# Performance work log

Hardware: AMD Instinct MI355X
Metric: run time of the kernel (lower is better)

## Reference

```python
import jax, jax.numpy as jnp
import numpy as np
from functools import partial

B, T, F = 4096, 256, 32
H1, H2, NT = 64, 32, 3


def _lstm_layer(x, W_ih, W_hh, b_ih, b_hh):
    """Torch-style LSTM (batch_first). x: [B,T,Fin], W_ih: [4H,Fin], W_hh: [4H,H].
    Gate order i, f, g, o. Returns all hidden states [B,T,H]."""
    Bsz = x.shape[0]
    H = W_hh.shape[1]
    # Precompute input contribution for all timesteps (one big GEMM)
    xg = jnp.einsum('btf,gf->btg', x, W_ih) + b_ih + b_hh  # [B,T,4H]

    def step(carry, xg_t):
        h, c = carry
        gates = xg_t + h @ W_hh.T  # [B,4H]
        i, f, g, o = jnp.split(gates, 4, axis=-1)
        i = jax.nn.sigmoid(i)
        f = jax.nn.sigmoid(f)
        g = jnp.tanh(g)
        o = jax.nn.sigmoid(o)
        c = f * c + i * g
        h = o * jnp.tanh(c)
        return (h, c), h

    init = (jnp.zeros((Bsz, H), x.dtype), jnp.zeros((Bsz, H), x.dtype))
    _, hs = jax.lax.scan(step, init, jnp.swapaxes(xg, 0, 1))  # hs: [T,B,H]
    return jnp.swapaxes(hs, 0, 1)


def setup_inputs() -> dict:
    key = jax.random.key(0)
    ks = jax.random.split(key, 12)
    s1 = 1.0 / np.sqrt(H1)
    s2 = 1.0 / np.sqrt(H2)
    u = lambda k, shape, s: jax.random.uniform(k, shape, jnp.float32, -s, s)
    return {
        'x': jax.random.normal(ks[0], (B, T, F), jnp.float32),
        'W_ih1': u(ks[1], (4 * H1, F), s1),
        'W_hh1': u(ks[2], (4 * H1, H1), s1),
        'b_ih1': u(ks[3], (4 * H1,), s1),
        'b_hh1': u(ks[4], (4 * H1,), s1),
        'W_ih2': u(ks[5], (4 * H2, H1), s2),
        'W_hh2': u(ks[6], (4 * H2, H2), s2),
        'b_ih2': u(ks[7], (4 * H2,), s2),
        'b_hh2': u(ks[8], (4 * H2,), s2),
        'W_head': u(ks[9], (NT, H2), s2),
        'b_head': u(ks[10], (NT,), s2),
    }


def reference(x, W_ih1, W_hh1, b_ih1, b_hh1, W_ih2, W_hh2, b_ih2, b_hh2, W_head, b_head):
    h1 = _lstm_layer(x, W_ih1, W_hh1, b_ih1, b_hh1)   # [B,T,64]; dropout is identity in eval
    h2 = _lstm_layer(h1, W_ih2, W_hh2, b_ih2, b_hh2)  # [B,T,32]
    last = h2[:, -1, :]                               # [B,32]
    return last @ W_head.T + b_head                   # [B,3]
```

## Files before the change

kernel.cpp:

```cpp
#include <hip/hip_runtime.h>

#define Bsz 4096
#define Tt  256
#define Ff  32
#define H1  64
#define H2  32
#define NTAPS 3
#define BT  8
#define NTHR 512
#define CH  16

typedef _Float16 half8  __attribute__((ext_vector_type(8)));
typedef __fp16   fp16x2 __attribute__((ext_vector_type(2)));
typedef float    f32x4  __attribute__((ext_vector_type(4)));

#define H1S 72
#define H2S 40
#define HDS 33

__device__ __forceinline__ float lstm_unit(float pi, float pf, float pg, float po,
                                           float& c) {
    const float K1 = 1.4426950408889634f;
    float ei = __builtin_amdgcn_exp2f(-K1 * pi);
    float ef = __builtin_amdgcn_exp2f(-K1 * pf);
    float eg = __builtin_amdgcn_exp2f(-2.0f * K1 * __builtin_fabsf(pg));
    float eo = __builtin_amdgcn_exp2f(-K1 * po);
    float p1 = (1.0f + ei) * (1.0f + eg);
    float pf1 = 1.0f + ef;
    float R  = __builtin_amdgcn_rcpf(p1 * pf1);
    float t1 = c * p1;
    float t2 = __builtin_copysignf(1.0f - eg, pg) * pf1;
    c = (t1 + t2) * R;
    float ec = __builtin_amdgcn_exp2f(-2.0f * K1 * __builtin_fabsf(c));
    float th = (1.0f - ec) * __builtin_amdgcn_rcpf((1.0f + eo) * (1.0f + ec));
    return __builtin_copysignf(th, c);
}

#define MFMA16(a, b, c) __builtin_amdgcn_mfma_f32_16x16x32_f16((a), (b), (c), 0, 0, 0)

__device__ __forceinline__ void dma16(const float* gp, const float* lp) {
    __builtin_amdgcn_global_load_lds(
        (const __attribute__((address_space(1))) void*)gp,
        (__attribute__((address_space(3))) void*)lp, 16, 0, 0);
}

__device__ __forceinline__ half8 cvt8(f32x4 lo, f32x4 hi) {
    union { half8 v; fp16x2 h[4]; } ax;
    ax.h[0] = __builtin_amdgcn_cvt_pkrtz(lo[0], lo[1]);
    ax.h[1] = __builtin_amdgcn_cvt_pkrtz(lo[2], lo[3]);
    ax.h[2] = __builtin_amdgcn_cvt_pkrtz(hi[0], hi[1]);
    ax.h[3] = __builtin_amdgcn_cvt_pkrtz(hi[2], hi[3]);
    return ax.v;
}

__global__ __launch_bounds__(NTHR, 2)
void lstm2_fused(const float* __restrict__ x,
                 const float* __restrict__ Wih1, const float* __restrict__ Whh1,
                 const float* __restrict__ bih1, const float* __restrict__ bhh1,
                 const float* __restrict__ Wih2, const float* __restrict__ Whh2,
                 const float* __restrict__ bih2, const float* __restrict__ bhh2,
                 const float* __restrict__ Whead, const float* __restrict__ bhead,
                 float* __restrict__ out)
{
    __shared__ __align__(16) _Float16 sH1[2][BT][H1S];
    __shared__ __align__(16) _Float16 sH2[2][BT][H2S];
    __shared__ __align__(16) float    sXC[2][CH][8][BT][4];
    __shared__ __align__(16) float    sHead[BT][HDS];

    const int tid  = threadIdx.x;
    const int wid  = tid >> 6;
    const int lane = tid & 63;
    const int l15  = lane & 15;
    const int q    = lane >> 4;
    const int row8 = l15 & 7;
    const int b0   = blockIdx.x * BT;
    const int u    = wid & 3;
    const bool isL1 = (wid < 4);

    const int colL1 = u * 16 + l15;
    const int r0  = (q >> 1) * 2, r1v = r0 + 1;
    const int bLo = (q & 1) * 4 + (q >> 1) * 2;
    const int hT = u & 1, rh = u >> 1;
    const int rL2 = (q >> 1) * 2 + rh;
    const int bL2 = (q & 1) * 4 + (q >> 1) * 2 + rh;

    const int bL  = lane & 7;
    const int f4L = lane >> 3;
    const float* gbase = x + (size_t)(b0 + bL) * Tt * Ff + f4L * 4;

    if (!isL1) {
        #pragma unroll
        for (int j = 0; j < 4; ++j) {
            int tl = u * 4 + j;
            dma16(gbase + (size_t)tl * Ff, &sXC[0][tl][0][0][0]);
        }
    }

    half8 wH[4][3];
    float bias[4];
    if (isL1) {
        #pragma unroll
        for (int G = 0; G < 4; ++G) {
            int gr = G * 64 + colL1;
            #pragma unroll
            for (int c = 0; c < 2; ++c) {
                half8 v;
                #pragma unroll
                for (int e = 0; e < 8; ++e)
                    v[e] = (_Float16)Whh1[gr * H1 + c * 32 + q * 8 + e];
                wH[G][c] = v;
            }
            half8 vx;
            #pragma unroll
            for (int e = 0; e < 8; ++e)
                vx[e] = (_Float16)Wih1[gr * Ff + q * 8 + e];
            wH[G][2] = vx;
            bias[G] = bih1[gr] + bhh1[gr];
        }
    } else {
        #pragma unroll
        for (int G = 0; G < 4; ++G) {
            int gr2 = G * 32 + hT * 16 + l15;
            half8 v0, v1, v2;
            #pragma unroll
            for (int e = 0; e < 8; ++e) {
                int k = q * 8 + e;
                v0[e] = (_Float16)Whh2[gr2 * H2 + k];
                v1[e] = (_Float16)Wih2[gr2 * H1 + k];
                v2[e] = (_Float16)Wih2[gr2 * H1 + 32 + k];
            }
            wH[G][0] = v0; wH[G][1] = v1; wH[G][2] = v2;
            bias[G] = bih2[gr2] + bhh2[gr2];
        }
    }

    for (int idx = tid; idx < BT * H1S; idx += NTHR) ((_Float16*)sH1[1])[idx] = (_Float16)0.0f;
    for (int idx = tid; idx < BT * H2S; idx += NTHR) ((_Float16*)sH2[1])[idx] = (_Float16)0.0f;

    __syncthreads();

    f32x4 xgN[4];
    if (isL1) {
        f32x4 lo = *(const f32x4*)&sXC[0][0][2 * q][row8][0];
        f32x4 hi = *(const f32x4*)&sXC[0][0][2 * q + 1][row8][0];
        half8 ax = cvt8(lo, hi);
        #pragma unroll
        for (int G = 0; G < 4; ++G) {
            f32x4 a = {bias[G], bias[G], bias[G], bias[G]};
            xgN[G] = MFMA16(ax, wH[G][2], a);
        }
    }

    float cs0 = 0.0f, cs1 = 0.0f;

    #pragma unroll 2
    for (int i = 0; i < Tt; ++i) {
        const int cur = i & 1, nxt = cur ^ 1;
        const int cbuf = (i >> 4) & 1;

        if (!isL1 && (i & (CH - 1)) == 0 && i + CH < Tt) {
            const float* gb = gbase + (size_t)(i + CH) * Ff;
            #pragma unroll
            for (int j = 0; j < 4; ++j) {
                int tl = u * 4 + j;
                dma16(gb + (size_t)tl * Ff, &sXC[cbuf ^ 1][tl][0][0][0]);
            }
        }

        half8 a0 = *(const half8*)&sH1[nxt][row8][q * 8];
        half8 a1 = *(const half8*)&sH1[nxt][row8][32 + q * 8];

        if (isL1) {
            f32x4 acc[4];
            #pragma unroll
            for (int G = 0; G < 4; ++G) {
                f32x4 a = xgN[G];
                a = MFMA16(a0, wH[G][0], a);
                a = MFMA16(a1, wH[G][1], a);
                acc[G] = a;
            }
            float h0  = lstm_unit(acc[0][r0],  acc[1][r0],  acc[2][r0],  acc[3][r0],  cs0);
            float h1v = lstm_unit(acc[0][r1v], acc[1][r1v], acc[2][r1v], acc[3][r1v], cs1);
            sH1[cur][bLo][colL1]     = (_Float16)h0;
            sH1[cur][bLo + 1][colL1] = (_Float16)h1v;

            if (i + 1 < Tt) {
                const int t = i + 1, cb = (t >> 4) & 1, t16 = t & (CH - 1);
                f32x4 lo = *(const f32x4*)&sXC[cb][t16][2 * q][row8][0];
                f32x4 hi = *(const f32x4*)&sXC[cb][t16][2 * q + 1][row8][0];
                half8 ax = cvt8(lo, hi);
                #pragma unroll
                for (int G = 0; G < 4; ++G) {
                    f32x4 a = {bias[G], bias[G], bias[G], bias[G]};
                    xgN[G] = MFMA16(ax, wH[G][2], a);
                }
            }
        } else if (i >= 1) {
            half8 ah = *(const half8*)&sH2[cur][row8][q * 8];
            f32x4 acc[4];
            #pragma unroll
            for (int G = 0; G < 4; ++G) {
                f32x4 a = {bias[G], bias[G], bias[G], bias[G]};
                a = MFMA16(ah, wH[G][0], a);
                a = MFMA16(a0, wH[G][1], a);
                a = MFMA16(a1, wH[G][2], a);
                acc[G] = a;
            }
            float hA = lstm_unit(acc[0][rL2], acc[1][rL2], acc[2][rL2], acc[3][rL2], cs0);
            sH2[nxt][bL2][hT * 16 + l15] = (_Float16)hA;
        }

        __syncthreads();
    }

    {
        const int cur = Tt & 1;
        const int nxt = cur ^ 1;
        if (!isL1) {
            half8 a0 = *(const half8*)&sH1[nxt][row8][q * 8];
            half8 a1 = *(const half8*)&sH1[nxt][row8][32 + q * 8];
            half8 ah = *(const half8*)&sH2[cur][row8][q * 8];
            f32x4 acc[4];
            #pragma unroll
            for (int G = 0; G < 4; ++G) {
                f32x4 a = {bias[G], bias[G], bias[G], bias[G]};
                a = MFMA16(ah, wH[G][0], a);
                a = MFMA16(a0, wH[G][1], a);
                a = MFMA16(a1, wH[G][2], a);
                acc[G] = a;
            }
            float hA = lstm_unit(acc[0][rL2], acc[1][rL2], acc[2][rL2], acc[3][rL2], cs0);
            sHead[bL2][hT * 16 + l15] = hA;
        }
        __syncthreads();
    }

    if (tid < BT * NTAPS) {
        int b = tid / NTAPS, n = tid - b * NTAPS;
        float s = bhead[n];
        #pragma unroll
        for (int k = 0; k < H2; ++k) s = fmaf(sHead[b][k], Whead[n * H2 + k], s);
        out[(size_t)(b0 + b) * NTAPS + n] = s;
    }
}

extern "C" void kernel_launch(void* const* d_in, const int* in_sizes, int n_in,
                              void* d_out, int out_size, void* d_ws, size_t ws_size,
                              hipStream_t stream) {
    const float* xp    = (const float*)d_in[0];
    const float* Wih1  = (const float*)d_in[1];
    const float* Whh1  = (const float*)d_in[2];
    const float* bih1  = (const float*)d_in[3];
    const float* bhh1  = (const float*)d_in[4];
    const float* Wih2  = (const float*)d_in[5];
    const float* Whh2  = (const float*)d_in[6];
    const float* bih2  = (const float*)d_in[7];
    const float* bhh2  = (const float*)d_in[8];
    const float* Whead = (const float*)d_in[9];
    const float* bhead = (const float*)d_in[10];
    float* outp = (float*)d_out;

    hipLaunchKernelGGL(lstm2_fused, dim3(Bsz / BT), dim3(NTHR), 0, stream,
                       xp, Wih1, Whh1, bih1, bhh1, Wih2, Whh2, bih2, bhh2,
                       Whead, bhead, outp);
}
```

Measured before the change: 383.0 us.

## Load x directly into registers with two-step prefetch and reblock hidden-state LDS layout

Drops the chunked global-to-LDS DMA staging of x done by the layer-2 waves. Each layer-1 lane now reads its own x slice from global memory into registers, prefetched two timesteps ahead with A/B double buffering. The hidden-state LDS arrays are also reorganised into [k-block][batch][8] tiles so each half8 read is a contiguous 16 bytes, which should cut bank conflicts. The trade-off is that global-load latency now sits on the layer-1 recurrence path and depends on the prefetch distance being enough, and layer-1 waves need more registers.

```diff
diff --git a/kernel.cpp b/kernel.cpp
--- a/kernel.cpp
+++ b/kernel.cpp
@@ -8,15 +8,11 @@
 #define NTAPS 3
 #define BT  8
 #define NTHR 512
-#define CH  16
+#define HDS 33
 
 typedef _Float16 half8  __attribute__((ext_vector_type(8)));
 typedef __fp16   fp16x2 __attribute__((ext_vector_type(2)));
 typedef float    f32x4  __attribute__((ext_vector_type(4)));
-
-#define H1S 72
-#define H2S 40
-#define HDS 33
 
 __device__ __forceinline__ float lstm_unit(float pi, float pf, float pg, float po,
                                            float& c) {
@@ -38,12 +34,6 @@
 
 #define MFMA16(a, b, c) __builtin_amdgcn_mfma_f32_16x16x32_f16((a), (b), (c), 0, 0, 0)
 
-__device__ __forceinline__ void dma16(const float* gp, const float* lp) {
-    __builtin_amdgcn_global_load_lds(
-        (const __attribute__((address_space(1))) void*)gp,
-        (__attribute__((address_space(3))) void*)lp, 16, 0, 0);
-}
-
 __device__ __forceinline__ half8 cvt8(f32x4 lo, f32x4 hi) {
     union { half8 v; fp16x2 h[4]; } ax;
     ax.h[0] = __builtin_amdgcn_cvt_pkrtz(lo[0], lo[1]);
@@ -62,9 +52,8 @@
                  const float* __restrict__ Whead, const float* __restrict__ bhead,
                  float* __restrict__ out)
 {
-    __shared__ __align__(16) _Float16 sH1[2][BT][H1S];
-    __shared__ __align__(16) _Float16 sH2[2][BT][H2S];
-    __shared__ __align__(16) float    sXC[2][CH][8][BT][4];
+    __shared__ __align__(16) _Float16 sH1f[2][8][BT][8];
+    __shared__ __align__(16) _Float16 sH2f[2][4][BT][8];
     __shared__ __align__(16) float    sHead[BT][HDS];
 
     const int tid  = threadIdx.x;
@@ -80,21 +69,14 @@
     const int colL1 = u * 16 + l15;
     const int r0  = (q >> 1) * 2, r1v = r0 + 1;
     const int bLo = (q & 1) * 4 + (q >> 1) * 2;
+    const int kb1 = colL1 >> 3, sb1 = colL1 & 7;
     const int hT = u & 1, rh = u >> 1;
     const int rL2 = (q >> 1) * 2 + rh;
     const int bL2 = (q & 1) * 4 + (q >> 1) * 2 + rh;
-
-    const int bL  = lane & 7;
-    const int f4L = lane >> 3;
-    const float* gbase = x + (size_t)(b0 + bL) * Tt * Ff + f4L * 4;
-
-    if (!isL1) {
-        #pragma unroll
-        for (int j = 0; j < 4; ++j) {
-            int tl = u * 4 + j;
-            dma16(gbase + (size_t)tl * Ff, &sXC[0][tl][0][0][0]);
-        }
-    }
+    const int col2 = hT * 16 + l15;
+    const int kb2 = col2 >> 3, sb2 = col2 & 7;
+
+    const float* gx = x + (size_t)(b0 + row8) * Tt * Ff + q * 8;
 
     half8 wH[4][3];
     float bias[4];
@@ -120,7 +102,7 @@
     } else {
         #pragma unroll
         for (int G = 0; G < 4; ++G) {
-            int gr2 = G * 32 + hT * 16 + l15;
+            int gr2 = G * 32 + col2;
             half8 v0, v1, v2;
             #pragma unroll
             for (int e = 0; e < 8; ++e) {
@@ -134,43 +116,42 @@
         }
     }
 
-    for (int idx = tid; idx < BT * H1S; idx += NTHR) ((_Float16*)sH1[1])[idx] = (_Float16)0.0f;
-    for (int idx = tid; idx < BT * H2S; idx += NTHR) ((_Float16*)sH2[1])[idx] = (_Float16)0.0f;
-
-    __syncthreads();
+    for (int idx = tid; idx < 2 * 8 * BT * 8; idx += NTHR) ((_Float16*)sH1f)[idx] = (_Float16)0.0f;
+    for (int idx = tid; idx < 2 * 4 * BT * 8; idx += NTHR) ((_Float16*)sH2f)[idx] = (_Float16)0.0f;
 
     f32x4 xgN[4];
+    f32x4 xA_lo, xA_hi, xB_lo, xB_hi;
     if (isL1) {
-        f32x4 lo = *(const f32x4*)&sXC[0][0][2 * q][row8][0];
-        f32x4 hi = *(const f32x4*)&sXC[0][0][2 * q + 1][row8][0];
+        f32x4 lo = *(const f32x4*)(gx);
+        f32x4 hi = *(const f32x4*)(gx + 4);
         half8 ax = cvt8(lo, hi);
         #pragma unroll
         for (int G = 0; G < 4; ++G) {
             f32x4 a = {bias[G], bias[G], bias[G], bias[G]};
             xgN[G] = MFMA16(ax, wH[G][2], a);
         }
-    }
+        xA_lo = *(const f32x4*)(gx + Ff);
+        xA_hi = *(const f32x4*)(gx + Ff + 4);
+    }
+
+    __syncthreads();
 
     float cs0 = 0.0f, cs1 = 0.0f;
 
     #pragma unroll 2
     for (int i = 0; i < Tt; ++i) {
         const int cur = i & 1, nxt = cur ^ 1;
-        const int cbuf = (i >> 4) & 1;
-
-        if (!isL1 && (i & (CH - 1)) == 0 && i + CH < Tt) {
-            const float* gb = gbase + (size_t)(i + CH) * Ff;
-            #pragma unroll
-            for (int j = 0; j < 4; ++j) {
-                int tl = u * 4 + j;
-                dma16(gb + (size_t)tl * Ff, &sXC[cbuf ^ 1][tl][0][0][0]);
-            }
-        }
-
-        half8 a0 = *(const half8*)&sH1[nxt][row8][q * 8];
-        half8 a1 = *(const half8*)&sH1[nxt][row8][32 + q * 8];
+
+        half8 a0 = *(const half8*)&sH1f[nxt][q][row8][0];
+        half8 a1 = *(const half8*)&sH1f[nxt][4 + q][row8][0];
 
         if (isL1) {
+            if (i + 2 < Tt) {
+                const float* gp = gx + (size_t)(i + 2) * Ff;
+                if (cur == 0) { xB_lo = *(const f32x4*)gp; xB_hi = *(const f32x4*)(gp + 4); }
+                else          { xA_lo = *(const f32x4*)gp; xA_hi = *(const f32x4*)(gp + 4); }
+            }
+
             f32x4 acc[4];
             #pragma unroll
             for (int G = 0; G < 4; ++G) {
@@ -181,14 +162,11 @@
             }
             float h0  = lstm_unit(acc[0][r0],  acc[1][r0],  acc[2][r0],  acc[3][r0],  cs0);
             float h1v = lstm_unit(acc[0][r1v], acc[1][r1v], acc[2][r1v], acc[3][r1v], cs1);
-            sH1[cur][bLo][colL1]     = (_Float16)h0;
-            sH1[cur][bLo + 1][colL1] = (_Float16)h1v;
+            sH1f[cur][kb1][bLo][sb1]     = (_Float16)h0;
+            sH1f[cur][kb1][bLo + 1][sb1] = (_Float16)h1v;
 
             if (i + 1 < Tt) {
-                const int t = i + 1, cb = (t >> 4) & 1, t16 = t & (CH - 1);
-                f32x4 lo = *(const f32x4*)&sXC[cb][t16][2 * q][row8][0];
-                f32x4 hi = *(const f32x4*)&sXC[cb][t16][2 * q + 1][row8][0];
-                half8 ax = cvt8(lo, hi);
+                half8 ax = (cur == 0) ? cvt8(xA_lo, xA_hi) : cvt8(xB_lo, xB_hi);
                 #pragma unroll
                 for (int G = 0; G < 4; ++G) {
                     f32x4 a = {bias[G], bias[G], bias[G], bias[G]};
@@ -196,7 +174,7 @@
                 }
             }
         } else if (i >= 1) {
-            half8 ah = *(const half8*)&sH2[cur][row8][q * 8];
+            half8 ah = *(const half8*)&sH2f[cur][q][row8][0];
             f32x4 acc[4];
             #pragma unroll
             for (int G = 0; G < 4; ++G) {
@@ -207,7 +185,7 @@
                 acc[G] = a;
             }
             float hA = lstm_unit(acc[0][rL2], acc[1][rL2], acc[2][rL2], acc[3][rL2], cs0);
-            sH2[nxt][bL2][hT * 16 + l15] = (_Float16)hA;
+            sH2f[nxt][kb2][bL2][sb2] = (_Float16)hA;
         }
 
         __syncthreads();
@@ -217,9 +195,9 @@
         const int cur = Tt & 1;
         const int nxt = cur ^ 1;
         if (!isL1) {
-            half8 a0 = *(const half8*)&sH1[nxt][row8][q * 8];
-            half8 a1 = *(const half8*)&sH1[nxt][row8][32 + q * 8];
-            half8 ah = *(const half8*)&sH2[cur][row8][q * 8];
+            half8 a0 = *(const half8*)&sH1f[nxt][q][row8][0];
+            half8 a1 = *(const half8*)&sH1f[nxt][4 + q][row8][0];
+            half8 ah = *(const half8*)&sH2f[cur][q][row8][0];
             f32x4 acc[4];
             #pragma unroll
             for (int G = 0; G < 4; ++G) {
@@ -230,7 +208,7 @@
                 acc[G] = a;
             }
             float hA = lstm_unit(acc[0][rL2], acc[1][rL2], acc[2][rL2], acc[3][rL2], cs0);
-            sHead[bL2][hT * 16 + l15] = hA;
+            sHead[bL2][col2] = hA;
         }
         __syncthreads();
     }
```

Measured after the change: 496.5 us. +29.6%, slower.
